# Optimization experiments

Hardware: AMD Instinct MI355X
Metric: run time of the kernel (lower is better)

## Reference

```python
import jax, jax.numpy as jnp
import numpy as np

HIDDEN = 4096
FFN = 14336
GS = 64  # groupsize


def dequant2(qw, scales, zeros, N):
    """Unpack 2-bit HQQ weights. qw: (N//4, K) int32, scales/zeros: (G, K).
    Returns W of shape (N, K) float: (bits - zeros[n % G]) * scales[n % G]."""
    G = scales.shape[0]
    n = jnp.arange(N)
    packed = qw[n // 4]                      # (N, K)
    shift = ((3 - (n % 4)) * 2).astype(qw.dtype)  # per-row bit shift
    vals = (packed >> shift[:, None]) & 3    # (N, K) 2-bit codes
    g = n % G
    return (vals.astype(scales.dtype) - zeros[g]) * scales[g]


def setup_inputs() -> dict:
    key = jax.random.key(0)
    ks = jax.random.split(key, 12)
    x = jax.random.normal(ks[0], (512, HIDDEN), dtype=jnp.float32)
    qw1 = jax.random.randint(ks[1], (FFN // 4, HIDDEN), 0, 256, dtype=jnp.int32)
    qw3 = jax.random.randint(ks[2], (FFN // 4, HIDDEN), 0, 256, dtype=jnp.int32)
    qw2 = jax.random.randint(ks[3], (HIDDEN // 4, FFN), 0, 256, dtype=jnp.int32)
    G1 = FFN // GS
    G2 = HIDDEN // GS
    s1 = jax.random.uniform(ks[4], (G1, HIDDEN), dtype=jnp.float32) * 0.05
    z1 = jax.random.uniform(ks[5], (G1, HIDDEN), dtype=jnp.float32)
    s3 = jax.random.uniform(ks[6], (G1, HIDDEN), dtype=jnp.float32) * 0.05
    z3 = jax.random.uniform(ks[7], (G1, HIDDEN), dtype=jnp.float32)
    s2 = jax.random.uniform(ks[8], (G2, FFN), dtype=jnp.float32) * 0.05
    z2 = jax.random.uniform(ks[9], (G2, FFN), dtype=jnp.float32)
    return {"x": x, "qw1": qw1, "s1": s1, "z1": z1, "qw3": qw3, "s3": s3,
            "z3": z3, "qw2": qw2, "s2": s2, "z2": z2, "groupsize": GS}


def reference(x, qw1, s1, z1, qw3, s3, z3, qw2, s2, z2, groupsize):
    # gate / up projections: C = x @ W^T, W dequantized to (N, K)
    w1 = dequant2(qw1, s1, z1, FFN)      # (FFN, HIDDEN)
    w3 = dequant2(qw3, s3, z3, FFN)      # (FFN, HIDDEN)
    w2 = dequant2(qw2, s2, z2, HIDDEN)   # (HIDDEN, FFN)
    gate = jnp.einsum('mk,nk->mn', x, w1)   # (M, FFN)
    up = jnp.einsum('mk,nk->mn', x, w3)     # (M, FFN)
    h = jax.nn.silu(gate) * up               # SwiGLU
    out = jnp.einsum('mf,hf->mh', h, w2)     # (M, HIDDEN)
    return out
```

## Files before the change

### kernel.cpp

```cpp
#include <hip/hip_runtime.h>
#include <hip/hip_fp16.h>
#include <stdint.h>

#define HIDDEN 4096
#define FFN    14336
#define MDIM   512
#define G1     224
#define G2     64
#define BK     64

typedef _Float16 f16x8 __attribute__((ext_vector_type(8)));
typedef float f32x4 __attribute__((ext_vector_type(4)));

__device__ __forceinline__ void gl_lds16(const void* g, void* l) {
    __builtin_amdgcn_global_load_lds(
        (const __attribute__((address_space(1))) uint32_t*)g,
        (__attribute__((address_space(3))) uint32_t*)l, 16, 0, 0);
}

#define SCHED0() __builtin_amdgcn_sched_barrier(0);


__global__ void cvt_x_kernel(const float* __restrict__ x, ushort* __restrict__ xb) {
    int i = blockIdx.x * blockDim.x + threadIdx.x;
    float4 v = ((const float4*)x)[i];
    __half2 a = __floats2half2_rn(v.x, v.y);
    __half2 b = __floats2half2_rn(v.z, v.w);
    ((uint2*)xb)[i] = make_uint2(__builtin_bit_cast(uint32_t, a),
                                 __builtin_bit_cast(uint32_t, b));
}

__global__ void build_sz_kernel(const float* __restrict__ s, const float* __restrict__ z,
                                uint32_t* __restrict__ outp) {
    int i = blockIdx.x * blockDim.x + threadIdx.x;
    float s0 = s[2 * i], s1 = s[2 * i + 1];
    float z0 = z[2 * i], z1 = z[2 * i + 1];
    __half2 hs = __floats2half2_rn(s0, s1);
    __half2 hn = __floats2half2_rn(-z0 * s0, -z1 * s1);
    ((uint2*)outp)[i] = make_uint2(__builtin_bit_cast(uint32_t, hs),
                                   __builtin_bit_cast(uint32_t, hn));
}

__device__ __forceinline__ uint32_t deq2(uint32_t w0, uint32_t w1, uint32_t sh,
                                         uint32_t spair, uint32_t npair) {
    uint32_t c0 = (w0 >> sh) & 3u;
    uint32_t c1 = (w1 >> sh) & 3u;
    uint32_t sel = 0x01000100u + c0 * 0x0202u + c1 * 0x02020000u;
    uint32_t codes = __builtin_amdgcn_perm(0x42004000u, 0x3C000000u, sel);
    __half2 r = __hfma2(__builtin_bit_cast(__half2, codes),
                        __builtin_bit_cast(__half2, spair),
                        __builtin_bit_cast(__half2, npair));
    return __builtin_bit_cast(uint32_t, r);
}


__global__ __launch_bounds__(256, 2)
void gemm_gateup(const ushort* __restrict__ xb, const uint32_t* __restrict__ qw1,
                 const uint32_t* __restrict__ sz1, const uint32_t* __restrict__ qw3,
                 const uint32_t* __restrict__ sz3, ushort* __restrict__ hbuf) {
    __shared__ ushort sAl[2][256 * 64];
    __shared__ ushort sB1[2][32 * 64];
    __shared__ ushort sB2[2][32 * 64];

    const int tid = threadIdx.x;
    const int idx = ((blockIdx.x & 7) * 112) + (blockIdx.x >> 3);
    const int mt = idx & 1, nt = idx >> 1;
    const int m0 = mt * 256, n0 = nt * 32;

    const int lane = tid & 63, w = tid >> 6;
    const int wm = w * 64;
    const int frow = lane & 15, fk = (lane >> 4) * 8;
    const int sw = (frow & 7) << 3;

    const int qs = (lane & 7) ^ ((lane >> 3) & 7);
    const ushort* apS[8];
#pragma unroll
    for (int s = 0; s < 8; ++s) {
        int r = s * 32 + w * 8 + (lane >> 3);
        apS[s] = xb + (size_t)(m0 + r) * HIDDEN + qs * 8;
    }

    const int bi = tid & 127;
    const int rp = bi >> 3;
    const int kc = (bi & 7) * 8;
    const int row0 = rp * 2;
    const int g0 = (n0 + row0) % G1;
    const uint32_t* qp = (tid < 128 ? qw1 : qw3) + (size_t)(n0 / 4 + (rp >> 1)) * HIDDEN + kc;
    const uint32_t* zp = (tid < 128 ? sz1 : sz3) + (size_t)g0 * HIDDEN + kc;
    ushort (*sB)[32 * 64] = (tid < 128) ? sB1 : sB2;
    const uint32_t sh0 = 6u - 4u * (uint32_t)(rp & 1);

    f32x4 accG[4][2], accU[4][2];
#pragma unroll
    for (int i = 0; i < 4; ++i)
#pragma unroll
        for (int j = 0; j < 2; ++j) {
            accG[i][j] = (f32x4){0.f, 0.f, 0.f, 0.f};
            accU[i][j] = (f32x4){0.f, 0.f, 0.f, 0.f};
        }

    uint4 pwA0, pwA1, pzA0, pzA1, pzA2, pzA3;
    uint4 pwB0, pwB1, pzB0, pzB1, pzB2, pzB3;

#define GU_GLDA(k0d, wbuf)                                                     \
    { _Pragma("unroll")                                                        \
      for (int s = 0; s < 8; ++s)                                              \
          gl_lds16(apS[s] + (k0d), &sAl[wbuf][(s * 256 + w * 64) * 8]); }

#define GU_LD(PW0, PW1, PZ0, PZ1, PZ2, PZ3, k0q)                               \
    PW0 = *(const uint4*)(qp + (k0q));                                         \
    PW1 = *(const uint4*)(qp + (k0q) + 4);                                     \
    PZ0 = *(const uint4*)(zp + (k0q));                                         \
    PZ1 = *(const uint4*)(zp + (k0q) + 4);                                     \
    PZ2 = *(const uint4*)(zp + HIDDEN + (k0q));                                \
    PZ3 = *(const uint4*)(zp + HIDDEN + (k0q) + 4);

#define GU_DEQ(wbuf, PW0, PW1, PZ0, PZ1, PZ2, PZ3)                             \
    { const uint32_t wv[8] = {(PW0).x, (PW0).y, (PW0).z, (PW0).w,              \
                              (PW1).x, (PW1).y, (PW1).z, (PW1).w};             \
      {   const uint32_t sp[4] = {(PZ0).x, (PZ0).z, (PZ1).x, (PZ1).z};         \
          const uint32_t np[4] = {(PZ0).y, (PZ0).w, (PZ1).y, (PZ1).w};         \
          uint32_t o[4];                                                       \
          _Pragma("unroll")                                                    \
          for (int j = 0; j < 4; ++j)                                          \
              o[j] = deq2(wv[2*j], wv[2*j+1], sh0, sp[j], np[j]);              \
          *(uint4*)&sB[wbuf][row0 * 64 + (kc ^ ((row0 & 7) << 3))] =           \
              make_uint4(o[0], o[1], o[2], o[3]);                              \
      }                                                                        \
      {   const uint32_t sp[4] = {(PZ2).x, (PZ2).z, (PZ3).x, (PZ3).z};         \
          const uint32_t np[4] = {(PZ2).y, (PZ2).w, (PZ3).y, (PZ3).w};         \
          uint32_t o[4];                                                       \
          _Pragma("unroll")                                                    \
          for (int j = 0; j < 4; ++j)                                          \
              o[j] = deq2(wv[2*j], wv[2*j+1], sh0 - 2u, sp[j], np[j]);         \
          const int row1 = row0 + 1;                                           \
          *(uint4*)&sB[wbuf][row1 * 64 + (kc ^ ((row1 & 7) << 3))] =           \
              make_uint4(o[0], o[1], o[2], o[3]);                              \
      } }

#define GU_COMP(rbuf)                                                          \
    { _Pragma("unroll")                                                        \
      for (int kk = 0; kk < 2; ++kk) {                                         \
          const int col = ((kk * 32) + fk) ^ sw;                               \
          f16x8 af[4], bg[2], bu[2];                                           \
          _Pragma("unroll")                                                    \
          for (int i = 0; i < 4; ++i)                                          \
              af[i] = *(const f16x8*)&sAl[rbuf][(wm + i * 16 + frow) * 64 + col]; \
          bg[0] = *(const f16x8*)&sB1[rbuf][frow * 64 + col];                  \
          bg[1] = *(const f16x8*)&sB1[rbuf][(16 + frow) * 64 + col];           \
          bu[0] = *(const f16x8*)&sB2[rbuf][frow * 64 + col];                  \
          bu[1] = *(const f16x8*)&sB2[rbuf][(16 + frow) * 64 + col];           \
          _Pragma("unroll")                                                    \
          for (int mi = 0; mi < 4; ++mi)                                       \
              _Pragma("unroll")                                                \
              for (int ni = 0; ni < 2; ++ni) {                                 \
                  accG[mi][ni] = __builtin_amdgcn_mfma_f32_16x16x32_f16(af[mi], bg[ni], accG[mi][ni], 0, 0, 0); \
                  accU[mi][ni] = __builtin_amdgcn_mfma_f32_16x16x32_f16(af[mi], bu[ni], accU[mi][ni], 0, 0, 0); \
              } } }

#define GU_STEP(k0s, WBUF, RBUF, PW0, PW1, PZ0, PZ1, PZ2, PZ3, DOPF, VMS)      \
    { GU_GLDA((k0s) + BK, WBUF) SCHED0()                                       \
      GU_DEQ(WBUF, PW0, PW1, PZ0, PZ1, PZ2, PZ3)                               \
      if (DOPF) { GU_LD(PW0, PW1, PZ0, PZ1, PZ2, PZ3, (k0s) + 3 * BK) }        \
      GU_COMP(RBUF)                                                            \
      asm volatile("s_waitcnt vmcnt(" VMS ") lgkmcnt(0)" ::: "memory");        \
      __builtin_amdgcn_s_barrier();                                            \
      SCHED0() }

    GU_GLDA(0, 0)
    GU_LD(pwA0, pwA1, pzA0, pzA1, pzA2, pzA3, 0)
    asm volatile("s_waitcnt vmcnt(0)" ::: "memory"); SCHED0()
    GU_DEQ(0, pwA0, pwA1, pzA0, pzA1, pzA2, pzA3)
    GU_LD(pwA0, pwA1, pzA0, pzA1, pzA2, pzA3, BK)
    GU_LD(pwB0, pwB1, pzB0, pzB1, pzB2, pzB3, 2 * BK)
    asm volatile("s_waitcnt lgkmcnt(0)" ::: "memory");
    __builtin_amdgcn_s_barrier();
    SCHED0()

    for (int t = 0; t < 60; t += 2) {
        GU_STEP(t * BK,       1, 0, pwA0, pwA1, pzA0, pzA1, pzA2, pzA3, 1, "6")
        GU_STEP((t + 1) * BK, 0, 1, pwB0, pwB1, pzB0, pzB1, pzB2, pzB3, 1, "6")
    }
    GU_STEP(60 * BK, 1, 0, pwA0, pwA1, pzA0, pzA1, pzA2, pzA3, 1, "6")
    GU_STEP(61 * BK, 0, 1, pwB0, pwB1, pzB0, pzB1, pzB2, pzB3, 0, "0")
    GU_STEP(62 * BK, 1, 0, pwA0, pwA1, pzA0, pzA1, pzA2, pzA3, 0, "0")
    GU_COMP(1)

    ushort* so = &sAl[0][0];
    const int rb = (lane >> 4) * 4, cb = lane & 15;
#pragma unroll
    for (int mi = 0; mi < 4; ++mi)
#pragma unroll
        for (int ni = 0; ni < 2; ++ni) {
            f32x4 g = accG[mi][ni], u = accU[mi][ni];
            const int row = wm + mi * 16 + rb;
            const int colx = ni * 16 + cb;
#pragma unroll
            for (int r = 0; r < 4; ++r) {
                float gv = g[r];
                float hv = __fdividef(gv, 1.0f + __expf(-gv)) * u[r];
                __half hh = __float2half(hv);
                so[(row + r) * 32 + colx] = __builtin_bit_cast(ushort, hh);
            }
        }
    __syncthreads();
    {
        ushort* dst = hbuf + (size_t)(m0 + tid) * FFN + n0;
        const ushort* src = so + tid * 32;
#pragma unroll
        for (int i = 0; i < 4; ++i)
            *(uint4*)(dst + 8 * i) = *(const uint4*)(src + 8 * i);
    }
#undef GU_GLDA
#undef GU_LD
#undef GU_DEQ
#undef GU_COMP
#undef GU_STEP
}


__global__ __launch_bounds__(256, 2)
void gemm_down(const ushort* __restrict__ hb, const uint32_t* __restrict__ qw2,
               const uint32_t* __restrict__ sz2, float* __restrict__ part) {
    __shared__ ushort sAl[2][256 * 64];
    __shared__ ushort sBd[2][32 * 64];

    const int tid = threadIdx.x;
    const int idx = ((blockIdx.x & 7) * 64) + (blockIdx.x >> 3);
    const int mt = idx & 1, nt = (idx >> 1) & 127, sk = idx >> 8;
    const int m0 = mt * 256, n0 = nt * 32;
    const int kbeg = sk * (FFN / 2);

    const int lane = tid & 63, w = tid >> 6;
    const int wm = w * 64;
    const int frow = lane & 15, fk = (lane >> 4) * 8;
    const int sw = (frow & 7) << 3;

    const int qs = (lane & 7) ^ ((lane >> 3) & 7);
    const ushort* apS[8];
#pragma unroll
    for (int s = 0; s < 8; ++s) {
        int r = s * 32 + w * 8 + (lane >> 3);
        apS[s] = hb + (size_t)(m0 + r) * FFN + kbeg + qs * 8;
    }

    const int r = tid >> 3;
    const int kc = (tid & 7) * 8;
    const int g = ((nt & 1) * 32) + r;
    const uint32_t* qp = qw2 + (size_t)(n0 / 4 + (r >> 2)) * FFN + kbeg + kc;
    const uint32_t* zp = sz2 + (size_t)g * FFN + kbeg + kc;
    const uint32_t sh = 6u - 2u * (uint32_t)(r & 3);

    f32x4 acc[4][2];
#pragma unroll
    for (int i = 0; i < 4; ++i)
#pragma unroll
        for (int j = 0; j < 2; ++j) acc[i][j] = (f32x4){0.f, 0.f, 0.f, 0.f};

    uint4 pwA0, pwA1, pzA0, pzA1;
    uint4 pwB0, pwB1, pzB0, pzB1;

#define GD_GLDA(k0d, wbuf)                                                     \
    { _Pragma("unroll")                                                        \
      for (int s = 0; s < 8; ++s)                                              \
          gl_lds16(apS[s] + (k0d), &sAl[wbuf][(s * 256 + w * 64) * 8]); }

#define GD_LD(PW0, PW1, PZ0, PZ1, k0q)                                         \
    PW0 = *(const uint4*)(qp + (k0q));                                         \
    PW1 = *(const uint4*)(qp + (k0q) + 4);                                     \
    PZ0 = *(const uint4*)(zp + (k0q));                                         \
    PZ1 = *(const uint4*)(zp + (k0q) + 4);

#define GD_DEQ(wbuf, PW0, PW1, PZ0, PZ1)                                       \
    { const uint32_t wv[8] = {(PW0).x, (PW0).y, (PW0).z, (PW0).w,              \
                              (PW1).x, (PW1).y, (PW1).z, (PW1).w};             \
      const uint32_t sp[4] = {(PZ0).x, (PZ0).z, (PZ1).x, (PZ1).z};             \
      const uint32_t np[4] = {(PZ0).y, (PZ0).w, (PZ1).y, (PZ1).w};             \
      uint32_t o[4];                                                           \
      _Pragma("unroll")                                                        \
      for (int j = 0; j < 4; ++j)                                              \
          o[j] = deq2(wv[2*j], wv[2*j+1], sh, sp[j], np[j]);                   \
      *(uint4*)&sBd[wbuf][r * 64 + (kc ^ ((r & 7) << 3))] =                    \
          make_uint4(o[0], o[1], o[2], o[3]); }

#define GD_COMP(rbuf)                                                          \
    { _Pragma("unroll")                                                        \
      for (int kk = 0; kk < 2; ++kk) {                                         \
          const int col = ((kk * 32) + fk) ^ sw;                               \
          f16x8 af[4], bf[2];                                                  \
          _Pragma("unroll")                                                    \
          for (int i = 0; i < 4; ++i)                                          \
              af[i] = *(const f16x8*)&sAl[rbuf][(wm + i * 16 + frow) * 64 + col]; \
          bf[0] = *(const f16x8*)&sBd[rbuf][frow * 64 + col];                  \
          bf[1] = *(const f16x8*)&sBd[rbuf][(16 + frow) * 64 + col];           \
          _Pragma("unroll")                                                    \
          for (int mi = 0; mi < 4; ++mi)                                       \
              _Pragma("unroll")                                                \
              for (int ni = 0; ni < 2; ++ni)                                   \
                  acc[mi][ni] = __builtin_amdgcn_mfma_f32_16x16x32_f16(af[mi], bf[ni], acc[mi][ni], 0, 0, 0); \
      } }

#define GD_STEP(k0s, WBUF, RBUF, PW0, PW1, PZ0, PZ1, DOPF, VMS)                \
    { GD_GLDA((k0s) + BK, WBUF) SCHED0()                                       \
      GD_DEQ(WBUF, PW0, PW1, PZ0, PZ1)                                         \
      if (DOPF) { GD_LD(PW0, PW1, PZ0, PZ1, (k0s) + 3 * BK) }                  \
      GD_COMP(RBUF)                                                            \
      asm volatile("s_waitcnt vmcnt(" VMS ") lgkmcnt(0)" ::: "memory");        \
      __builtin_amdgcn_s_barrier();                                            \
      SCHED0() }

    GD_GLDA(0, 0)
    GD_LD(pwA0, pwA1, pzA0, pzA1, 0)
    asm volatile("s_waitcnt vmcnt(0)" ::: "memory"); SCHED0()
    GD_DEQ(0, pwA0, pwA1, pzA0, pzA1)
    GD_LD(pwA0, pwA1, pzA0, pzA1, BK)
    GD_LD(pwB0, pwB1, pzB0, pzB1, 2 * BK)
    asm volatile("s_waitcnt lgkmcnt(0)" ::: "memory");
    __builtin_amdgcn_s_barrier();
    SCHED0()

    for (int t = 0; t < 108; t += 2) {
        GD_STEP(t * BK,       1, 0, pwA0, pwA1, pzA0, pzA1, 1, "4")
        GD_STEP((t + 1) * BK, 0, 1, pwB0, pwB1, pzB0, pzB1, 1, "4")
    }
    GD_STEP(108 * BK, 1, 0, pwA0, pwA1, pzA0, pzA1, 1, "4")
    GD_STEP(109 * BK, 0, 1, pwB0, pwB1, pzB0, pzB1, 0, "0")
    GD_STEP(110 * BK, 1, 0, pwA0, pwA1, pzA0, pzA1, 0, "0")
    GD_COMP(1)

    float* pp = part + (size_t)sk * MDIM * HIDDEN;
    const int rb = (lane >> 4) * 4, cb = lane & 15;
#pragma unroll
    for (int mi = 0; mi < 4; ++mi)
#pragma unroll
        for (int ni = 0; ni < 2; ++ni) {
            f32x4 a = acc[mi][ni];
            const int mm = m0 + wm + mi * 16 + rb;
            const int nn = n0 + ni * 16 + cb;
#pragma unroll
            for (int rr = 0; rr < 4; ++rr) pp[(size_t)(mm + rr) * HIDDEN + nn] = a[rr];
        }
#undef GD_GLDA
#undef GD_LD
#undef GD_DEQ
#undef GD_COMP
#undef GD_STEP
}


__global__ void reduce_out(const float* __restrict__ part, float* __restrict__ out) {
    int i = blockIdx.x * blockDim.x + threadIdx.x;
    const int Q = MDIM * HIDDEN / 4;
    float4 a = ((const float4*)part)[i];
    float4 b = ((const float4*)part)[i + Q];
    float4 o;
    o.x = a.x + b.x; o.y = a.y + b.y; o.z = a.z + b.z; o.w = a.w + b.w;
    ((float4*)out)[i] = o;
}


extern "C" void kernel_launch(void* const* d_in, const int* in_sizes, int n_in,
                              void* d_out, int out_size, void* d_ws, size_t ws_size,
                              hipStream_t stream) {
    (void)in_sizes; (void)n_in; (void)out_size; (void)ws_size;

    const float* x  = (const float*)d_in[0];
    const uint32_t* qw1 = (const uint32_t*)d_in[1];
    const float* s1 = (const float*)d_in[2];
    const float* z1 = (const float*)d_in[3];
    const uint32_t* qw3 = (const uint32_t*)d_in[4];
    const float* s3 = (const float*)d_in[5];
    const float* z3 = (const float*)d_in[6];
    const uint32_t* qw2 = (const uint32_t*)d_in[7];
    const float* s2 = (const float*)d_in[8];
    const float* z2 = (const float*)d_in[9];
    float* out = (float*)d_out;

    char* ws = (char*)d_ws;
    ushort*   xb   = (ushort*)ws;
    uint32_t* szp1 = (uint32_t*)(ws + (size_t)MDIM * HIDDEN * 2);
    uint32_t* szp3 = szp1 + (size_t)G1 * HIDDEN;
    uint32_t* szp2 = szp3 + (size_t)G1 * HIDDEN;
    ushort*   hbuf = (ushort*)(szp2 + (size_t)G2 * FFN);
    float*    part = (float*)((char*)hbuf + (size_t)MDIM * FFN * 2);

    cvt_x_kernel<<<(MDIM * HIDDEN / 4) / 256, 256, 0, stream>>>(x, xb);
    build_sz_kernel<<<(G1 * HIDDEN / 2) / 256, 256, 0, stream>>>(s1, z1, szp1);
    build_sz_kernel<<<(G1 * HIDDEN / 2) / 256, 256, 0, stream>>>(s3, z3, szp3);
    build_sz_kernel<<<(G2 * FFN / 2) / 256, 256, 0, stream>>>(s2, z2, szp2);

    gemm_gateup<<<(FFN / 32) * (MDIM / 256), 256, 0, stream>>>(xb, qw1, szp1, qw3, szp3, hbuf);
    gemm_down<<<2 * (MDIM / 256) * (HIDDEN / 32), 256, 0, stream>>>(hbuf, qw2, szp2, part);
    reduce_out<<<(MDIM * HIDDEN / 4) / 256, 256, 0, stream>>>(part, out);
}
```

Measured before the change: 335.4 us.

## Load A fragments directly from global into registers, drop LDS A staging

Both GEMM kernels stop staging the activation tile through LDS via global_load_lds and instead load MFMA A fragments straight from global memory into registers each step. Scale/zero loads move inline into the dequant step, and the register prefetch depth for weights shrinks to one stage. This frees LDS so occupancy bounds rise to 4 blocks/CU, and gemm_down drops to a 128-row M tile with twice the blocks. The cost is uncoalesced, latency-exposed global A loads with no software pipelining, plus reduced A reuse per block in the down projection.

Result: slower. 675.4 us (+101.4%).

```diff
diff --git a/kernel.cpp b/kernel.cpp
--- a/kernel.cpp
+++ b/kernel.cpp
@@ -12,13 +12,11 @@
 typedef _Float16 f16x8 __attribute__((ext_vector_type(8)));
 typedef float f32x4 __attribute__((ext_vector_type(4)));
 
-__device__ __forceinline__ void gl_lds16(const void* g, void* l) {
-    __builtin_amdgcn_global_load_lds(
-        (const __attribute__((address_space(1))) uint32_t*)g,
-        (__attribute__((address_space(3))) uint32_t*)l, 16, 0, 0);
-}
-
 #define SCHED0() __builtin_amdgcn_sched_barrier(0);
+#define LGKM_BAR()                                            \
+    asm volatile("s_waitcnt lgkmcnt(0)" ::: "memory");        \
+    __builtin_amdgcn_s_barrier();                             \
+    __builtin_amdgcn_sched_barrier(0);
 
 
 __global__ void cvt_x_kernel(const float* __restrict__ x, ushort* __restrict__ xb) {
@@ -54,13 +52,13 @@
 }
 
 
-__global__ __launch_bounds__(256, 2)
+__global__ __launch_bounds__(256, 4)
 void gemm_gateup(const ushort* __restrict__ xb, const uint32_t* __restrict__ qw1,
                  const uint32_t* __restrict__ sz1, const uint32_t* __restrict__ qw3,
                  const uint32_t* __restrict__ sz3, ushort* __restrict__ hbuf) {
-    __shared__ ushort sAl[2][256 * 64];
     __shared__ ushort sB1[2][32 * 64];
     __shared__ ushort sB2[2][32 * 64];
+    __shared__ ushort sE[256 * 32];
 
     const int tid = threadIdx.x;
     const int idx = ((blockIdx.x & 7) * 112) + (blockIdx.x >> 3);
@@ -72,13 +70,10 @@
     const int frow = lane & 15, fk = (lane >> 4) * 8;
     const int sw = (frow & 7) << 3;
 
-    const int qs = (lane & 7) ^ ((lane >> 3) & 7);
-    const ushort* apS[8];
-#pragma unroll
-    for (int s = 0; s < 8; ++s) {
-        int r = s * 32 + w * 8 + (lane >> 3);
-        apS[s] = xb + (size_t)(m0 + r) * HIDDEN + qs * 8;
-    }
+    uint32_t aoff[4];
+#pragma unroll
+    for (int i = 0; i < 4; ++i)
+        aoff[i] = (uint32_t)(m0 + wm + i * 16 + frow) * HIDDEN + fk;
 
     const int bi = tid & 127;
     const int rp = bi >> 3;
@@ -99,27 +94,21 @@
             accU[i][j] = (f32x4){0.f, 0.f, 0.f, 0.f};
         }
 
-    uint4 pwA0, pwA1, pzA0, pzA1, pzA2, pzA3;
-    uint4 pwB0, pwB1, pzB0, pzB1, pzB2, pzB3;
-
-#define GU_GLDA(k0d, wbuf)                                                     \
-    { _Pragma("unroll")                                                        \
-      for (int s = 0; s < 8; ++s)                                              \
-          gl_lds16(apS[s] + (k0d), &sAl[wbuf][(s * 256 + w * 64) * 8]); }
-
-#define GU_LD(PW0, PW1, PZ0, PZ1, PZ2, PZ3, k0q)                               \
-    PW0 = *(const uint4*)(qp + (k0q));                                         \
-    PW1 = *(const uint4*)(qp + (k0q) + 4);                                     \
-    PZ0 = *(const uint4*)(zp + (k0q));                                         \
-    PZ1 = *(const uint4*)(zp + (k0q) + 4);                                     \
-    PZ2 = *(const uint4*)(zp + HIDDEN + (k0q));                                \
-    PZ3 = *(const uint4*)(zp + HIDDEN + (k0q) + 4);
-
-#define GU_DEQ(wbuf, PW0, PW1, PZ0, PZ1, PZ2, PZ3)                             \
-    { const uint32_t wv[8] = {(PW0).x, (PW0).y, (PW0).z, (PW0).w,              \
-                              (PW1).x, (PW1).y, (PW1).z, (PW1).w};             \
-      {   const uint32_t sp[4] = {(PZ0).x, (PZ0).z, (PZ1).x, (PZ1).z};         \
-          const uint32_t np[4] = {(PZ0).y, (PZ0).w, (PZ1).y, (PZ1).w};         \
+    uint4 pw0, pw1;
+
+#define GU_LDQW(k0q)                                                           \
+    pw0 = *(const uint4*)(qp + (k0q));                                         \
+    pw1 = *(const uint4*)(qp + (k0q) + 4);
+
+#define GU_DEQ(wbuf, k0z)                                                      \
+    { uint4 pz0 = *(const uint4*)(zp + (k0z));                                 \
+      uint4 pz1 = *(const uint4*)(zp + (k0z) + 4);                             \
+      uint4 pz2 = *(const uint4*)(zp + HIDDEN + (k0z));                        \
+      uint4 pz3 = *(const uint4*)(zp + HIDDEN + (k0z) + 4);                    \
+      const uint32_t wv[8] = {pw0.x, pw0.y, pw0.z, pw0.w,                      \
+                              pw1.x, pw1.y, pw1.z, pw1.w};                     \
+      {   const uint32_t sp[4] = {pz0.x, pz0.z, pz1.x, pz1.z};                 \
+          const uint32_t np[4] = {pz0.y, pz0.w, pz1.y, pz1.w};                 \
           uint32_t o[4];                                                       \
           _Pragma("unroll")                                                    \
           for (int j = 0; j < 4; ++j)                                          \
@@ -127,8 +116,8 @@
           *(uint4*)&sB[wbuf][row0 * 64 + (kc ^ ((row0 & 7) << 3))] =           \
               make_uint4(o[0], o[1], o[2], o[3]);                              \
       }                                                                        \
-      {   const uint32_t sp[4] = {(PZ2).x, (PZ2).z, (PZ3).x, (PZ3).z};         \
-          const uint32_t np[4] = {(PZ2).y, (PZ2).w, (PZ3).y, (PZ3).w};         \
+      {   const uint32_t sp[4] = {pz2.x, pz2.z, pz3.x, pz3.z};                 \
+          const uint32_t np[4] = {pz2.y, pz2.w, pz3.y, pz3.w};                 \
           uint32_t o[4];                                                       \
           _Pragma("unroll")                                                    \
           for (int j = 0; j < 4; ++j)                                          \
@@ -138,55 +127,48 @@
               make_uint4(o[0], o[1], o[2], o[3]);                              \
       } }
 
-#define GU_COMP(rbuf)                                                          \
-    { _Pragma("unroll")                                                        \
+#define GU_COMP(rbuf, k0a)                                                     \
+    { f16x8 af0[4], af1[4];                                                    \
+      _Pragma("unroll")                                                        \
+      for (int i = 0; i < 4; ++i) {                                            \
+          af0[i] = *(const f16x8*)&xb[aoff[i] + (k0a)];                        \
+          af1[i] = *(const f16x8*)&xb[aoff[i] + (k0a) + 32];                   \
+      }                                                                        \
+      _Pragma("unroll")                                                        \
       for (int kk = 0; kk < 2; ++kk) {                                         \
           const int col = ((kk * 32) + fk) ^ sw;                               \
-          f16x8 af[4], bg[2], bu[2];                                           \
-          _Pragma("unroll")                                                    \
-          for (int i = 0; i < 4; ++i)                                          \
-              af[i] = *(const f16x8*)&sAl[rbuf][(wm + i * 16 + frow) * 64 + col]; \
+          f16x8 bg[2], bu[2];                                                  \
           bg[0] = *(const f16x8*)&sB1[rbuf][frow * 64 + col];                  \
           bg[1] = *(const f16x8*)&sB1[rbuf][(16 + frow) * 64 + col];           \
           bu[0] = *(const f16x8*)&sB2[rbuf][frow * 64 + col];                  \
           bu[1] = *(const f16x8*)&sB2[rbuf][(16 + frow) * 64 + col];           \
           _Pragma("unroll")                                                    \
-          for (int mi = 0; mi < 4; ++mi)                                       \
+          for (int mi = 0; mi < 4; ++mi) {                                     \
+              f16x8 a = kk ? af1[mi] : af0[mi];                                \
               _Pragma("unroll")                                                \
               for (int ni = 0; ni < 2; ++ni) {                                 \
-                  accG[mi][ni] = __builtin_amdgcn_mfma_f32_16x16x32_f16(af[mi], bg[ni], accG[mi][ni], 0, 0, 0); \
-                  accU[mi][ni] = __builtin_amdgcn_mfma_f32_16x16x32_f16(af[mi], bu[ni], accU[mi][ni], 0, 0, 0); \
-              } } }
-
-#define GU_STEP(k0s, WBUF, RBUF, PW0, PW1, PZ0, PZ1, PZ2, PZ3, DOPF, VMS)      \
-    { GU_GLDA((k0s) + BK, WBUF) SCHED0()                                       \
-      GU_DEQ(WBUF, PW0, PW1, PZ0, PZ1, PZ2, PZ3)                               \
-      if (DOPF) { GU_LD(PW0, PW1, PZ0, PZ1, PZ2, PZ3, (k0s) + 3 * BK) }        \
-      GU_COMP(RBUF)                                                            \
-      asm volatile("s_waitcnt vmcnt(" VMS ") lgkmcnt(0)" ::: "memory");        \
-      __builtin_amdgcn_s_barrier();                                            \
-      SCHED0() }
-
-    GU_GLDA(0, 0)
-    GU_LD(pwA0, pwA1, pzA0, pzA1, pzA2, pzA3, 0)
-    asm volatile("s_waitcnt vmcnt(0)" ::: "memory"); SCHED0()
-    GU_DEQ(0, pwA0, pwA1, pzA0, pzA1, pzA2, pzA3)
-    GU_LD(pwA0, pwA1, pzA0, pzA1, pzA2, pzA3, BK)
-    GU_LD(pwB0, pwB1, pzB0, pzB1, pzB2, pzB3, 2 * BK)
-    asm volatile("s_waitcnt lgkmcnt(0)" ::: "memory");
-    __builtin_amdgcn_s_barrier();
-    SCHED0()
-
-    for (int t = 0; t < 60; t += 2) {
-        GU_STEP(t * BK,       1, 0, pwA0, pwA1, pzA0, pzA1, pzA2, pzA3, 1, "6")
-        GU_STEP((t + 1) * BK, 0, 1, pwB0, pwB1, pzB0, pzB1, pzB2, pzB3, 1, "6")
+                  accG[mi][ni] = __builtin_amdgcn_mfma_f32_16x16x32_f16(a, bg[ni], accG[mi][ni], 0, 0, 0); \
+                  accU[mi][ni] = __builtin_amdgcn_mfma_f32_16x16x32_f16(a, bu[ni], accU[mi][ni], 0, 0, 0); \
+              } } } }
+
+#define GU_STEP(tcur, WBUF, RBUF, DOPF)                                        \
+    { GU_DEQ(WBUF, ((tcur) + 1) * BK)                                          \
+      if (DOPF) { GU_LDQW(((tcur) + 2) * BK) }                                 \
+      GU_COMP(RBUF, (tcur) * BK)                                               \
+      LGKM_BAR() }
+
+    GU_LDQW(0)
+    GU_DEQ(0, 0)
+    GU_LDQW(BK)
+    LGKM_BAR()
+
+    for (int t = 0; t < 62; t += 2) {
+        GU_STEP(t,     1, 0, 1)
+        GU_STEP(t + 1, 0, 1, 1)
     }
-    GU_STEP(60 * BK, 1, 0, pwA0, pwA1, pzA0, pzA1, pzA2, pzA3, 1, "6")
-    GU_STEP(61 * BK, 0, 1, pwB0, pwB1, pzB0, pzB1, pzB2, pzB3, 0, "0")
-    GU_STEP(62 * BK, 1, 0, pwA0, pwA1, pzA0, pzA1, pzA2, pzA3, 0, "0")
-    GU_COMP(1)
-
-    ushort* so = &sAl[0][0];
+    GU_STEP(62, 1, 0, 0)
+    GU_COMP(1, 63 * BK)
+
     const int rb = (lane >> 4) * 4, cb = lane & 15;
 #pragma unroll
     for (int mi = 0; mi < 4; ++mi)
@@ -200,49 +182,44 @@
                 float gv = g[r];
                 float hv = __fdividef(gv, 1.0f + __expf(-gv)) * u[r];
                 __half hh = __float2half(hv);
-                so[(row + r) * 32 + colx] = __builtin_bit_cast(ushort, hh);
+                sE[(row + r) * 32 + colx] = __builtin_bit_cast(ushort, hh);
             }
         }
     __syncthreads();
     {
         ushort* dst = hbuf + (size_t)(m0 + tid) * FFN + n0;
-        const ushort* src = so + tid * 32;
+        const ushort* src = sE + tid * 32;
 #pragma unroll
         for (int i = 0; i < 4; ++i)
             *(uint4*)(dst + 8 * i) = *(const uint4*)(src + 8 * i);
     }
-#undef GU_GLDA
-#undef GU_LD
+#undef GU_LDQW
 #undef GU_DEQ
 #undef GU_COMP
 #undef GU_STEP
 }
 
 
-__global__ __launch_bounds__(256, 2)
+__global__ __launch_bounds__(256, 4)
 void gemm_down(const ushort* __restrict__ hb, const uint32_t* __restrict__ qw2,
                const uint32_t* __restrict__ sz2, float* __restrict__ part) {
-    __shared__ ushort sAl[2][256 * 64];
     __shared__ ushort sBd[2][32 * 64];
 
     const int tid = threadIdx.x;
-    const int idx = ((blockIdx.x & 7) * 64) + (blockIdx.x >> 3);
-    const int mt = idx & 1, nt = (idx >> 1) & 127, sk = idx >> 8;
-    const int m0 = mt * 256, n0 = nt * 32;
+    const int idx = ((blockIdx.x & 7) * 128) + (blockIdx.x >> 3);
+    const int mt = idx & 3, nt = (idx >> 2) & 127, sk = idx >> 9;
+    const int m0 = mt * 128, n0 = nt * 32;
     const int kbeg = sk * (FFN / 2);
 
     const int lane = tid & 63, w = tid >> 6;
-    const int wm = w * 64;
+    const int wm = w * 32;
     const int frow = lane & 15, fk = (lane >> 4) * 8;
     const int sw = (frow & 7) << 3;
 
-    const int qs = (lane & 7) ^ ((lane >> 3) & 7);
-    const ushort* apS[8];
-#pragma unroll
-    for (int s = 0; s < 8; ++s) {
-        int r = s * 32 + w * 8 + (lane >> 3);
-        apS[s] = hb + (size_t)(m0 + r) * FFN + kbeg + qs * 8;
-    }
+    uint32_t aoff[2];
+#pragma unroll
+    for (int i = 0; i < 2; ++i)
+        aoff[i] = (uint32_t)(m0 + wm + i * 16 + frow) * FFN + kbeg + fk;
 
     const int r = tid >> 3;
     const int kc = (tid & 7) * 8;
@@ -251,31 +228,25 @@
     const uint32_t* zp = sz2 + (size_t)g * FFN + kbeg + kc;
     const uint32_t sh = 6u - 2u * (uint32_t)(r & 3);
 
-    f32x4 acc[4][2];
-#pragma unroll
-    for (int i = 0; i < 4; ++i)
+    f32x4 acc[2][2];
+#pragma unroll
+    for (int i = 0; i < 2; ++i)
 #pragma unroll
         for (int j = 0; j < 2; ++j) acc[i][j] = (f32x4){0.f, 0.f, 0.f, 0.f};
 
-    uint4 pwA0, pwA1, pzA0, pzA1;
-    uint4 pwB0, pwB1, pzB0, pzB1;
-
-#define GD_GLDA(k0d, wbuf)                                                     \
-    { _Pragma("unroll")                                                        \
-      for (int s = 0; s < 8; ++s)                                              \
-          gl_lds16(apS[s] + (k0d), &sAl[wbuf][(s * 256 + w * 64) * 8]); }
-
-#define GD_LD(PW0, PW1, PZ0, PZ1, k0q)                                         \
-    PW0 = *(const uint4*)(qp + (k0q));                                         \
-    PW1 = *(const uint4*)(qp + (k0q) + 4);                                     \
-    PZ0 = *(const uint4*)(zp + (k0q));                                         \
-    PZ1 = *(const uint4*)(zp + (k0q) + 4);
-
-#define GD_DEQ(wbuf, PW0, PW1, PZ0, PZ1)                                       \
-    { const uint32_t wv[8] = {(PW0).x, (PW0).y, (PW0).z, (PW0).w,              \
-                              (PW1).x, (PW1).y, (PW1).z, (PW1).w};             \
-      const uint32_t sp[4] = {(PZ0).x, (PZ0).z, (PZ1).x, (PZ1).z};             \
-      const uint32_t np[4] = {(PZ0).y, (PZ0).w, (PZ1).y, (PZ1).w};             \
+    uint4 pw0, pw1;
+
+#define GD_LDQW(k0q)                                                           \
+    pw0 = *(const uint4*)(qp + (k0q));                                         \
+    pw1 = *(const uint4*)(qp + (k0q) + 4);
+
+#define GD_DEQ(wbuf, k0z)                                                      \
+    { uint4 pz0 = *(const uint4*)(zp + (k0z));                                 \
+      uint4 pz1 = *(const uint4*)(zp + (k0z) + 4);                             \
+      const uint32_t wv[8] = {pw0.x, pw0.y, pw0.z, pw0.w,                      \
+                              pw1.x, pw1.y, pw1.z, pw1.w};                     \
+      const uint32_t sp[4] = {pz0.x, pz0.z, pz1.x, pz1.z};                     \
+      const uint32_t np[4] = {pz0.y, pz0.w, pz1.y, pz1.w};                     \
       uint32_t o[4];                                                           \
       _Pragma("unroll")                                                        \
       for (int j = 0; j < 4; ++j)                                              \
@@ -283,55 +254,49 @@
       *(uint4*)&sBd[wbuf][r * 64 + (kc ^ ((r & 7) << 3))] =                    \
           make_uint4(o[0], o[1], o[2], o[3]); }
 
-#define GD_COMP(rbuf)                                                          \
-    { _Pragma("unroll")                                                        \
+#define GD_COMP(rbuf, k0a)                                                     \
+    { f16x8 af0[2], af1[2];                                                    \
+      _Pragma("unroll")                                                        \
+      for (int i = 0; i < 2; ++i) {                                            \
+          af0[i] = *(const f16x8*)&hb[aoff[i] + (k0a)];                        \
+          af1[i] = *(const f16x8*)&hb[aoff[i] + (k0a) + 32];                   \
+      }                                                                        \
+      _Pragma("unroll")                                                        \
       for (int kk = 0; kk < 2; ++kk) {                                         \
           const int col = ((kk * 32) + fk) ^ sw;                               \
-          f16x8 af[4], bf[2];                                                  \
-          _Pragma("unroll")                                                    \
-          for (int i = 0; i < 4; ++i)                                          \
-              af[i] = *(const f16x8*)&sAl[rbuf][(wm + i * 16 + frow) * 64 + col]; \
+          f16x8 bf[2];                                                         \
           bf[0] = *(const f16x8*)&sBd[rbuf][frow * 64 + col];                  \
           bf[1] = *(const f16x8*)&sBd[rbuf][(16 + frow) * 64 + col];           \
           _Pragma("unroll")                                                    \
-          for (int mi = 0; mi < 4; ++mi)                                       \
+          for (int mi = 0; mi < 2; ++mi) {                                     \
+              f16x8 a = kk ? af1[mi] : af0[mi];                                \
               _Pragma("unroll")                                                \
               for (int ni = 0; ni < 2; ++ni)                                   \
-                  acc[mi][ni] = __builtin_amdgcn_mfma_f32_16x16x32_f16(af[mi], bf[ni], acc[mi][ni], 0, 0, 0); \
-      } }
-
-#define GD_STEP(k0s, WBUF, RBUF, PW0, PW1, PZ0, PZ1, DOPF, VMS)                \
-    { GD_GLDA((k0s) + BK, WBUF) SCHED0()                                       \
-      GD_DEQ(WBUF, PW0, PW1, PZ0, PZ1)                                         \
-      if (DOPF) { GD_LD(PW0, PW1, PZ0, PZ1, (k0s) + 3 * BK) }                  \
-      GD_COMP(RBUF)                                                            \
-      asm volatile("s_waitcnt vmcnt(" VMS ") lgkmcnt(0)" ::: "memory");        \
-      __builtin_amdgcn_s_barrier();                                            \
-      SCHED0() }
-
-    GD_GLDA(0, 0)
-    GD_LD(pwA0, pwA1, pzA0, pzA1, 0)
-    asm volatile("s_waitcnt vmcnt(0)" ::: "memory"); SCHED0()
-    GD_DEQ(0, pwA0, pwA1, pzA0, pzA1)
-    GD_LD(pwA0, pwA1, pzA0, pzA1, BK)
-    GD_LD(pwB0, pwB1, pzB0, pzB1, 2 * BK)
-    asm volatile("s_waitcnt lgkmcnt(0)" ::: "memory");
-    __builtin_amdgcn_s_barrier();
-    SCHED0()
-
-    for (int t = 0; t < 108; t += 2) {
-        GD_STEP(t * BK,       1, 0, pwA0, pwA1, pzA0, pzA1, 1, "4")
-        GD_STEP((t + 1) * BK, 0, 1, pwB0, pwB1, pzB0, pzB1, 1, "4")
+                  acc[mi][ni] = __builtin_amdgcn_mfma_f32_16x16x32_f16(a, bf[ni], acc[mi][ni], 0, 0, 0); \
+          } } }
+
+#define GD_STEP(tcur, WBUF, RBUF, DOPF)                                        \
+    { GD_DEQ(WBUF, ((tcur) + 1) * BK)                                          \
+      if (DOPF) { GD_LDQW(((tcur) + 2) * BK) }                                 \
+      GD_COMP(RBUF, (tcur) * BK)                                               \
+      LGKM_BAR() }
+
+    GD_LDQW(0)
+    GD_DEQ(0, 0)
+    GD_LDQW(BK)
+    LGKM_BAR()
+
+    for (int t = 0; t < 110; t += 2) {
+        GD_STEP(t,     1, 0, 1)
+        GD_STEP(t + 1, 0, 1, 1)
     }
-    GD_STEP(108 * BK, 1, 0, pwA0, pwA1, pzA0, pzA1, 1, "4")
-    GD_STEP(109 * BK, 0, 1, pwB0, pwB1, pzB0, pzB1, 0, "0")
-    GD_STEP(110 * BK, 1, 0, pwA0, pwA1, pzA0, pzA1, 0, "0")
-    GD_COMP(1)
+    GD_STEP(110, 1, 0, 0)
+    GD_COMP(1, 111 * BK)
 
     float* pp = part + (size_t)sk * MDIM * HIDDEN;
     const int rb = (lane >> 4) * 4, cb = lane & 15;
 #pragma unroll
-    for (int mi = 0; mi < 4; ++mi)
+    for (int mi = 0; mi < 2; ++mi)
 #pragma unroll
         for (int ni = 0; ni < 2; ++ni) {
             f32x4 a = acc[mi][ni];
@@ -340,8 +305,7 @@
 #pragma unroll
             for (int rr = 0; rr < 4; ++rr) pp[(size_t)(mm + rr) * HIDDEN + nn] = a[rr];
         }
-#undef GD_GLDA
-#undef GD_LD
+#undef GD_LDQW
 #undef GD_DEQ
 #undef GD_COMP
 #undef GD_STEP
@@ -390,6 +354,6 @@
     build_sz_kernel<<<(G2 * FFN / 2) / 256, 256, 0, stream>>>(s2, z2, szp2);
 
     gemm_gateup<<<(FFN / 32) * (MDIM / 256), 256, 0, stream>>>(xb, qw1, szp1, qw3, szp3, hbuf);
-    gemm_down<<<2 * (MDIM / 256) * (HIDDEN / 32), 256, 0, stream>>>(hbuf, qw2, szp2, part);
+    gemm_down<<<2 * (MDIM / 128) * (HIDDEN / 32), 256, 0, stream>>>(hbuf, qw2, szp2, part);
     reduce_out<<<(MDIM * HIDDEN / 4) / 256, 256, 0, stream>>>(part, out);
 }
```

## Prepack activations into MFMA fragment layout and load A directly to registers

Applied to the files above, without the earlier changes.

The x conversion and the gate/up epilogue now write activations in a fragment-packed layout of 16x32 tiles, so each lane's f16x8 operand sits contiguously. Both GEMMs then load A fragments from global memory straight into registers, double-buffered, instead of staging 256x64 A tiles through LDS with global_load_lds. This frees a large amount of LDS and removes the A-side LDS reads, which could raise occupancy and ease LDS bandwidth. In exchange it raises register pressure with 16 extra f16x8 values per thread, and relies on the loads landing in time without explicit vmcnt waits, since the barrier now waits only on lgkmcnt.

Measured after the change: 285.2 us (median of 2 runs). 15.0% less time.

```diff
diff --git a/kernel.cpp b/kernel.cpp
--- a/kernel.cpp
+++ b/kernel.cpp
@@ -8,26 +8,35 @@
 #define G1     224
 #define G2     64
 #define BK     64
+#define KB_H   128
+#define KB_F   448
 
 typedef _Float16 f16x8 __attribute__((ext_vector_type(8)));
 typedef float f32x4 __attribute__((ext_vector_type(4)));
 
-__device__ __forceinline__ void gl_lds16(const void* g, void* l) {
-    __builtin_amdgcn_global_load_lds(
-        (const __attribute__((address_space(1))) uint32_t*)g,
-        (__attribute__((address_space(3))) uint32_t*)l, 16, 0, 0);
-}
-
 #define SCHED0() __builtin_amdgcn_sched_barrier(0);
-
-
-__global__ void cvt_x_kernel(const float* __restrict__ x, ushort* __restrict__ xb) {
+#define LGKM_BAR()                                            \
+    asm volatile("s_waitcnt lgkmcnt(0)" ::: "memory");        \
+    __builtin_amdgcn_s_barrier();                             \
+    __builtin_amdgcn_sched_barrier(0);
+
+
+__global__ void cvt_xp_kernel(const float* __restrict__ x, ushort* __restrict__ xbp) {
     int i = blockIdx.x * blockDim.x + threadIdx.x;
-    float4 v = ((const float4*)x)[i];
-    __half2 a = __floats2half2_rn(v.x, v.y);
-    __half2 b = __floats2half2_rn(v.z, v.w);
-    ((uint2*)xb)[i] = make_uint2(__builtin_bit_cast(uint32_t, a),
-                                 __builtin_bit_cast(uint32_t, b));
+    int ls = i & 63;
+    int kb = (i >> 6) & (KB_H - 1);
+    int mb = i >> 13;
+    int row = mb * 16 + (ls & 15);
+    int col = kb * 32 + (ls >> 4) * 8;
+    const float4* src = (const float4*)&x[(size_t)row * HIDDEN + col];
+    float4 v0 = src[0], v1 = src[1];
+    __half2 h0 = __floats2half2_rn(v0.x, v0.y);
+    __half2 h1 = __floats2half2_rn(v0.z, v0.w);
+    __half2 h2 = __floats2half2_rn(v1.x, v1.y);
+    __half2 h3 = __floats2half2_rn(v1.z, v1.w);
+    uint4 o = make_uint4(__builtin_bit_cast(uint32_t, h0), __builtin_bit_cast(uint32_t, h1),
+                         __builtin_bit_cast(uint32_t, h2), __builtin_bit_cast(uint32_t, h3));
+    ((uint4*)xbp)[i] = o;
 }
 
 __global__ void build_sz_kernel(const float* __restrict__ s, const float* __restrict__ z,
@@ -55,12 +64,12 @@
 
 
 __global__ __launch_bounds__(256, 2)
-void gemm_gateup(const ushort* __restrict__ xb, const uint32_t* __restrict__ qw1,
+void gemm_gateup(const ushort* __restrict__ xbp, const uint32_t* __restrict__ qw1,
                  const uint32_t* __restrict__ sz1, const uint32_t* __restrict__ qw3,
-                 const uint32_t* __restrict__ sz3, ushort* __restrict__ hbuf) {
-    __shared__ ushort sAl[2][256 * 64];
+                 const uint32_t* __restrict__ sz3, ushort* __restrict__ hp) {
     __shared__ ushort sB1[2][32 * 64];
     __shared__ ushort sB2[2][32 * 64];
+    __shared__ ushort sE[256 * 32];
 
     const int tid = threadIdx.x;
     const int idx = ((blockIdx.x & 7) * 112) + (blockIdx.x >> 3);
@@ -72,13 +81,10 @@
     const int frow = lane & 15, fk = (lane >> 4) * 8;
     const int sw = (frow & 7) << 3;
 
-    const int qs = (lane & 7) ^ ((lane >> 3) & 7);
-    const ushort* apS[8];
-#pragma unroll
-    for (int s = 0; s < 8; ++s) {
-        int r = s * 32 + w * 8 + (lane >> 3);
-        apS[s] = xb + (size_t)(m0 + r) * HIDDEN + qs * 8;
-    }
+    uint32_t abase[4];
+#pragma unroll
+    for (int mi = 0; mi < 4; ++mi)
+        abase[mi] = (uint32_t)(((m0 >> 4) + w * 4 + mi) * KB_H) * 512 + lane * 8;
 
     const int bi = tid & 127;
     const int rp = bi >> 3;
@@ -99,13 +105,17 @@
             accU[i][j] = (f32x4){0.f, 0.f, 0.f, 0.f};
         }
 
+    f16x8 afA[8], afB[8];
     uint4 pwA0, pwA1, pzA0, pzA1, pzA2, pzA3;
     uint4 pwB0, pwB1, pzB0, pzB1, pzB2, pzB3;
 
-#define GU_GLDA(k0d, wbuf)                                                     \
+#define GU_LDA(AF, tt)                                                         \
     { _Pragma("unroll")                                                        \
-      for (int s = 0; s < 8; ++s)                                              \
-          gl_lds16(apS[s] + (k0d), &sAl[wbuf][(s * 256 + w * 64) * 8]); }
+      for (int mi = 0; mi < 4; ++mi)                                           \
+          _Pragma("unroll")                                                    \
+          for (int kk = 0; kk < 2; ++kk)                                       \
+              AF[mi * 2 + kk] =                                                \
+                  *(const f16x8*)&xbp[abase[mi] + (uint32_t)((tt) * 2 + kk) * 512]; }
 
 #define GU_LD(PW0, PW1, PZ0, PZ1, PZ2, PZ3, k0q)                               \
     PW0 = *(const uint4*)(qp + (k0q));                                         \
@@ -138,55 +148,45 @@
               make_uint4(o[0], o[1], o[2], o[3]);                              \
       } }
 
-#define GU_COMP(rbuf)                                                          \
+#define GU_COMP(AF, rbuf)                                                      \
     { _Pragma("unroll")                                                        \
       for (int kk = 0; kk < 2; ++kk) {                                         \
           const int col = ((kk * 32) + fk) ^ sw;                               \
-          f16x8 af[4], bg[2], bu[2];                                           \
-          _Pragma("unroll")                                                    \
-          for (int i = 0; i < 4; ++i)                                          \
-              af[i] = *(const f16x8*)&sAl[rbuf][(wm + i * 16 + frow) * 64 + col]; \
-          bg[0] = *(const f16x8*)&sB1[rbuf][frow * 64 + col];                  \
-          bg[1] = *(const f16x8*)&sB1[rbuf][(16 + frow) * 64 + col];           \
-          bu[0] = *(const f16x8*)&sB2[rbuf][frow * 64 + col];                  \
-          bu[1] = *(const f16x8*)&sB2[rbuf][(16 + frow) * 64 + col];           \
-          _Pragma("unroll")                                                    \
-          for (int mi = 0; mi < 4; ++mi)                                       \
-              _Pragma("unroll")                                                \
-              for (int ni = 0; ni < 2; ++ni) {                                 \
-                  accG[mi][ni] = __builtin_amdgcn_mfma_f32_16x16x32_f16(af[mi], bg[ni], accG[mi][ni], 0, 0, 0); \
-                  accU[mi][ni] = __builtin_amdgcn_mfma_f32_16x16x32_f16(af[mi], bu[ni], accU[mi][ni], 0, 0, 0); \
-              } } }
-
-#define GU_STEP(k0s, WBUF, RBUF, PW0, PW1, PZ0, PZ1, PZ2, PZ3, DOPF, VMS)      \
-    { GU_GLDA((k0s) + BK, WBUF) SCHED0()                                       \
+          f16x8 bg0 = *(const f16x8*)&sB1[rbuf][frow * 64 + col];              \
+          f16x8 bg1 = *(const f16x8*)&sB1[rbuf][(16 + frow) * 64 + col];       \
+          f16x8 bu0 = *(const f16x8*)&sB2[rbuf][frow * 64 + col];              \
+          f16x8 bu1 = *(const f16x8*)&sB2[rbuf][(16 + frow) * 64 + col];       \
+          _Pragma("unroll")                                                    \
+          for (int mi = 0; mi < 4; ++mi) {                                     \
+              accG[mi][0] = __builtin_amdgcn_mfma_f32_16x16x32_f16(AF[mi*2+kk], bg0, accG[mi][0], 0, 0, 0); \
+              accG[mi][1] = __builtin_amdgcn_mfma_f32_16x16x32_f16(AF[mi*2+kk], bg1, accG[mi][1], 0, 0, 0); \
+              accU[mi][0] = __builtin_amdgcn_mfma_f32_16x16x32_f16(AF[mi*2+kk], bu0, accU[mi][0], 0, 0, 0); \
+              accU[mi][1] = __builtin_amdgcn_mfma_f32_16x16x32_f16(AF[mi*2+kk], bu1, accU[mi][1], 0, 0, 0); \
+          } } }
+
+#define GU_STEP(tcur, AFW, AFR, WBUF, RBUF, PW0, PW1, PZ0, PZ1, PZ2, PZ3, DOLDA, DOLQ) \
+    { if (DOLDA) { GU_LDA(AFW, (tcur) + 1) } SCHED0()                          \
       GU_DEQ(WBUF, PW0, PW1, PZ0, PZ1, PZ2, PZ3)                               \
-      if (DOPF) { GU_LD(PW0, PW1, PZ0, PZ1, PZ2, PZ3, (k0s) + 3 * BK) }        \
-      GU_COMP(RBUF)                                                            \
-      asm volatile("s_waitcnt vmcnt(" VMS ") lgkmcnt(0)" ::: "memory");        \
-      __builtin_amdgcn_s_barrier();                                            \
-      SCHED0() }
-
-    GU_GLDA(0, 0)
+      if (DOLQ) { GU_LD(PW0, PW1, PZ0, PZ1, PZ2, PZ3, ((tcur) + 3) * BK) }     \
+      GU_COMP(AFR, RBUF)                                                       \
+      LGKM_BAR() }
+
     GU_LD(pwA0, pwA1, pzA0, pzA1, pzA2, pzA3, 0)
-    asm volatile("s_waitcnt vmcnt(0)" ::: "memory"); SCHED0()
+    GU_LDA(afA, 0)
     GU_DEQ(0, pwA0, pwA1, pzA0, pzA1, pzA2, pzA3)
     GU_LD(pwA0, pwA1, pzA0, pzA1, pzA2, pzA3, BK)
     GU_LD(pwB0, pwB1, pzB0, pzB1, pzB2, pzB3, 2 * BK)
-    asm volatile("s_waitcnt lgkmcnt(0)" ::: "memory");
-    __builtin_amdgcn_s_barrier();
-    SCHED0()
+    LGKM_BAR()
 
     for (int t = 0; t < 60; t += 2) {
-        GU_STEP(t * BK,       1, 0, pwA0, pwA1, pzA0, pzA1, pzA2, pzA3, 1, "6")
-        GU_STEP((t + 1) * BK, 0, 1, pwB0, pwB1, pzB0, pzB1, pzB2, pzB3, 1, "6")
+        GU_STEP(t,     afB, afA, 1, 0, pwA0, pwA1, pzA0, pzA1, pzA2, pzA3, 1, 1)
+        GU_STEP(t + 1, afA, afB, 0, 1, pwB0, pwB1, pzB0, pzB1, pzB2, pzB3, 1, 1)
     }
-    GU_STEP(60 * BK, 1, 0, pwA0, pwA1, pzA0, pzA1, pzA2, pzA3, 1, "6")
-    GU_STEP(61 * BK, 0, 1, pwB0, pwB1, pzB0, pzB1, pzB2, pzB3, 0, "0")
-    GU_STEP(62 * BK, 1, 0, pwA0, pwA1, pzA0, pzA1, pzA2, pzA3, 0, "0")
-    GU_COMP(1)
-
-    ushort* so = &sAl[0][0];
+    GU_STEP(60, afB, afA, 1, 0, pwA0, pwA1, pzA0, pzA1, pzA2, pzA3, 1, 1)
+    GU_STEP(61, afA, afB, 0, 1, pwB0, pwB1, pzB0, pzB1, pzB2, pzB3, 1, 0)
+    GU_STEP(62, afB, afA, 1, 0, pwA0, pwA1, pzA0, pzA1, pzA2, pzA3, 1, 0)
+    GU_COMP(afB, 1)
+
     const int rb = (lane >> 4) * 4, cb = lane & 15;
 #pragma unroll
     for (int mi = 0; mi < 4; ++mi)
@@ -200,18 +200,20 @@
                 float gv = g[r];
                 float hv = __fdividef(gv, 1.0f + __expf(-gv)) * u[r];
                 __half hh = __float2half(hv);
-                so[(row + r) * 32 + colx] = __builtin_bit_cast(ushort, hh);
+                sE[(row + r) * 32 + colx] = __builtin_bit_cast(ushort, hh);
             }
         }
     __syncthreads();
     {
-        ushort* dst = hbuf + (size_t)(m0 + tid) * FFN + n0;
-        const ushort* src = so + tid * 32;
-#pragma unroll
-        for (int i = 0; i < 4; ++i)
-            *(uint4*)(dst + 8 * i) = *(const uint4*)(src + 8 * i);
+#pragma unroll
+        for (int j = 0; j < 4; ++j) {
+            const int slot = tid + j * 256;
+            const int mbi = slot >> 6, ls = slot & 63;
+            uint4 v = *(const uint4*)&sE[(mbi * 16 + (ls & 15)) * 32 + (ls >> 4) * 8];
+            *(uint4*)&hp[(size_t)(((m0 >> 4) + mbi) * KB_F + nt) * 512 + ls * 8] = v;
+        }
     }
-#undef GU_GLDA
+#undef GU_LDA
 #undef GU_LD
 #undef GU_DEQ
 #undef GU_COMP
@@ -220,33 +222,30 @@
 
 
 __global__ __launch_bounds__(256, 2)
-void gemm_down(const ushort* __restrict__ hb, const uint32_t* __restrict__ qw2,
+void gemm_down(const ushort* __restrict__ hp, const uint32_t* __restrict__ qw2,
                const uint32_t* __restrict__ sz2, float* __restrict__ part) {
-    __shared__ ushort sAl[2][256 * 64];
     __shared__ ushort sBd[2][32 * 64];
 
     const int tid = threadIdx.x;
     const int idx = ((blockIdx.x & 7) * 64) + (blockIdx.x >> 3);
     const int mt = idx & 1, nt = (idx >> 1) & 127, sk = idx >> 8;
     const int m0 = mt * 256, n0 = nt * 32;
-    const int kbeg = sk * (FFN / 2);
+    const int kb0 = sk * 224;
 
     const int lane = tid & 63, w = tid >> 6;
     const int wm = w * 64;
     const int frow = lane & 15, fk = (lane >> 4) * 8;
     const int sw = (frow & 7) << 3;
 
-    const int qs = (lane & 7) ^ ((lane >> 3) & 7);
-    const ushort* apS[8];
-#pragma unroll
-    for (int s = 0; s < 8; ++s) {
-        int r = s * 32 + w * 8 + (lane >> 3);
-        apS[s] = hb + (size_t)(m0 + r) * FFN + kbeg + qs * 8;
-    }
+    uint32_t abase[4];
+#pragma unroll
+    for (int mi = 0; mi < 4; ++mi)
+        abase[mi] = (uint32_t)(((m0 >> 4) + w * 4 + mi) * KB_F + kb0) * 512 + lane * 8;
 
     const int r = tid >> 3;
     const int kc = (tid & 7) * 8;
     const int g = ((nt & 1) * 32) + r;
+    const int kbeg = sk * (FFN / 2);
     const uint32_t* qp = qw2 + (size_t)(n0 / 4 + (r >> 2)) * FFN + kbeg + kc;
     const uint32_t* zp = sz2 + (size_t)g * FFN + kbeg + kc;
     const uint32_t sh = 6u - 2u * (uint32_t)(r & 3);
@@ -257,13 +256,17 @@
 #pragma unroll
         for (int j = 0; j < 2; ++j) acc[i][j] = (f32x4){0.f, 0.f, 0.f, 0.f};
 
+    f16x8 afA[8], afB[8];
     uint4 pwA0, pwA1, pzA0, pzA1;
     uint4 pwB0, pwB1, pzB0, pzB1;
 
-#define GD_GLDA(k0d, wbuf)                                                     \
+#define GD_LDA(AF, tt)                                                         \
     { _Pragma("unroll")                                                        \
-      for (int s = 0; s < 8; ++s)                                              \
-          gl_lds16(apS[s] + (k0d), &sAl[wbuf][(s * 256 + w * 64) * 8]); }
+      for (int mi = 0; mi < 4; ++mi)                                           \
+          _Pragma("unroll")                                                    \
+          for (int kk = 0; kk < 2; ++kk)                                       \
+              AF[mi * 2 + kk] =                                                \
+                  *(const f16x8*)&hp[abase[mi] + (uint32_t)((tt) * 2 + kk) * 512]; }
 
 #define GD_LD(PW0, PW1, PZ0, PZ1, k0q)                                         \
     PW0 = *(const uint4*)(qp + (k0q));                                         \
@@ -283,50 +286,40 @@
       *(uint4*)&sBd[wbuf][r * 64 + (kc ^ ((r & 7) << 3))] =                    \
           make_uint4(o[0], o[1], o[2], o[3]); }
 
-#define GD_COMP(rbuf)                                                          \
+#define GD_COMP(AF, rbuf)                                                      \
     { _Pragma("unroll")                                                        \
       for (int kk = 0; kk < 2; ++kk) {                                         \
           const int col = ((kk * 32) + fk) ^ sw;                               \
-          f16x8 af[4], bf[2];                                                  \
-          _Pragma("unroll")                                                    \
-          for (int i = 0; i < 4; ++i)                                          \
-              af[i] = *(const f16x8*)&sAl[rbuf][(wm + i * 16 + frow) * 64 + col]; \
-          bf[0] = *(const f16x8*)&sBd[rbuf][frow * 64 + col];                  \
-          bf[1] = *(const f16x8*)&sBd[rbuf][(16 + frow) * 64 + col];           \
-          _Pragma("unroll")                                                    \
-          for (int mi = 0; mi < 4; ++mi)                                       \
-              _Pragma("unroll")                                                \
-              for (int ni = 0; ni < 2; ++ni)                                   \
-                  acc[mi][ni] = __builtin_amdgcn_mfma_f32_16x16x32_f16(af[mi], bf[ni], acc[mi][ni], 0, 0, 0); \
-      } }
-
-#define GD_STEP(k0s, WBUF, RBUF, PW0, PW1, PZ0, PZ1, DOPF, VMS)                \
-    { GD_GLDA((k0s) + BK, WBUF) SCHED0()                                       \
+          f16x8 bf0 = *(const f16x8*)&sBd[rbuf][frow * 64 + col];              \
+          f16x8 bf1 = *(const f16x8*)&sBd[rbuf][(16 + frow) * 64 + col];       \
+          _Pragma("unroll")                                                    \
+          for (int mi = 0; mi < 4; ++mi) {                                     \
+              acc[mi][0] = __builtin_amdgcn_mfma_f32_16x16x32_f16(AF[mi*2+kk], bf0, acc[mi][0], 0, 0, 0); \
+              acc[mi][1] = __builtin_amdgcn_mfma_f32_16x16x32_f16(AF[mi*2+kk], bf1, acc[mi][1], 0, 0, 0); \
+          } } }
+
+#define GD_STEP(tcur, AFW, AFR, WBUF, RBUF, PW0, PW1, PZ0, PZ1, DOLDA, DOLQ)   \
+    { if (DOLDA) { GD_LDA(AFW, (tcur) + 1) } SCHED0()                          \
       GD_DEQ(WBUF, PW0, PW1, PZ0, PZ1)                                         \
-      if (DOPF) { GD_LD(PW0, PW1, PZ0, PZ1, (k0s) + 3 * BK) }                  \
-      GD_COMP(RBUF)                                                            \
-      asm volatile("s_waitcnt vmcnt(" VMS ") lgkmcnt(0)" ::: "memory");        \
-      __builtin_amdgcn_s_barrier();                                            \
-      SCHED0() }
-
-    GD_GLDA(0, 0)
+      if (DOLQ) { GD_LD(PW0, PW1, PZ0, PZ1, ((tcur) + 3) * BK) }               \
+      GD_COMP(AFR, RBUF)                                                       \
+      LGKM_BAR() }
+
     GD_LD(pwA0, pwA1, pzA0, pzA1, 0)
-    asm volatile("s_waitcnt vmcnt(0)" ::: "memory"); SCHED0()
+    GD_LDA(afA, 0)
     GD_DEQ(0, pwA0, pwA1, pzA0, pzA1)
     GD_LD(pwA0, pwA1, pzA0, pzA1, BK)
     GD_LD(pwB0, pwB1, pzB0, pzB1, 2 * BK)
-    asm volatile("s_waitcnt lgkmcnt(0)" ::: "memory");
-    __builtin_amdgcn_s_barrier();
-    SCHED0()
+    LGKM_BAR()
 
     for (int t = 0; t < 108; t += 2) {
-        GD_STEP(t * BK,       1, 0, pwA0, pwA1, pzA0, pzA1, 1, "4")
-        GD_STEP((t + 1) * BK, 0, 1, pwB0, pwB1, pzB0, pzB1, 1, "4")
+        GD_STEP(t,     afB, afA, 1, 0, pwA0, pwA1, pzA0, pzA1, 1, 1)
+        GD_STEP(t + 1, afA, afB, 0, 1, pwB0, pwB1, pzB0, pzB1, 1, 1)
     }
-    GD_STEP(108 * BK, 1, 0, pwA0, pwA1, pzA0, pzA1, 1, "4")
-    GD_STEP(109 * BK, 0, 1, pwB0, pwB1, pzB0, pzB1, 0, "0")
-    GD_STEP(110 * BK, 1, 0, pwA0, pwA1, pzA0, pzA1, 0, "0")
-    GD_COMP(1)
+    GD_STEP(108, afB, afA, 1, 0, pwA0, pwA1, pzA0, pzA1, 1, 1)
+    GD_STEP(109, afA, afB, 0, 1, pwB0, pwB1, pzB0, pzB1, 1, 0)
+    GD_STEP(110, afB, afA, 1, 0, pwA0, pwA1, pzA0, pzA1, 1, 0)
+    GD_COMP(afB, 1)
 
     float* pp = part + (size_t)sk * MDIM * HIDDEN;
     const int rb = (lane >> 4) * 4, cb = lane & 15;
@@ -340,7 +333,7 @@
 #pragma unroll
             for (int rr = 0; rr < 4; ++rr) pp[(size_t)(mm + rr) * HIDDEN + nn] = a[rr];
         }
-#undef GD_GLDA
+#undef GD_LDA
 #undef GD_LD
 #undef GD_DEQ
 #undef GD_COMP
@@ -377,19 +370,19 @@
     float* out = (float*)d_out;
 
     char* ws = (char*)d_ws;
-    ushort*   xb   = (ushort*)ws;
+    ushort*   xbp  = (ushort*)ws;
     uint32_t* szp1 = (uint32_t*)(ws + (size_t)MDIM * HIDDEN * 2);
     uint32_t* szp3 = szp1 + (size_t)G1 * HIDDEN;
     uint32_t* szp2 = szp3 + (size_t)G1 * HIDDEN;
-    ushort*   hbuf = (ushort*)(szp2 + (size_t)G2 * FFN);
-    float*    part = (float*)((char*)hbuf + (size_t)MDIM * FFN * 2);
-
-    cvt_x_kernel<<<(MDIM * HIDDEN / 4) / 256, 256, 0, stream>>>(x, xb);
+    ushort*   hp   = (ushort*)(szp2 + (size_t)G2 * FFN);
+    float*    part = (float*)((char*)hp + (size_t)MDIM * FFN * 2);
+
+    cvt_xp_kernel<<<(MDIM * HIDDEN / 8) / 256, 256, 0, stream>>>(x, xbp);
     build_sz_kernel<<<(G1 * HIDDEN / 2) / 256, 256, 0, stream>>>(s1, z1, szp1);
     build_sz_kernel<<<(G1 * HIDDEN / 2) / 256, 256, 0, stream>>>(s3, z3, szp3);
     build_sz_kernel<<<(G2 * FFN / 2) / 256, 256, 0, stream>>>(s2, z2, szp2);
 
-    gemm_gateup<<<(FFN / 32) * (MDIM / 256), 256, 0, stream>>>(xb, qw1, szp1, qw3, szp3, hbuf);
-    gemm_down<<<2 * (MDIM / 256) * (HIDDEN / 32), 256, 0, stream>>>(hbuf, qw2, szp2, part);
+    gemm_gateup<<<(FFN / 32) * (MDIM / 256), 256, 0, stream>>>(xbp, qw1, szp1, qw3, szp3, hp);
+    gemm_down<<<2 * (MDIM / 256) * (HIDDEN / 32), 256, 0, stream>>>(hp, qw2, szp2, part);
     reduce_out<<<(MDIM * HIDDEN / 4) / 256, 256, 0, stream>>>(part, out);
 }
```
